# Optimization experiments

Hardware: AMD Instinct MI355X
Metric: run time of the kernel (lower is better)

## Reference

```python
import jax, jax.numpy as jnp
import numpy as np

MARGIN = 4.1
TOPK = 100          # argsort(...)[:100] in the original mining loop
NORM_EPS = 1e-8     # F.cosine_similarity eps
B, C, H, W = 4, 256, 64, 64


def setup_inputs() -> dict:
    key = jax.random.key(0)
    k1, k2, k3 = jax.random.split(key, 3)
    return {
        "sketch_query_vectors": jax.random.normal(k1, (B, C, H, W), jnp.float32),
        "ref_key_vectors": jax.random.normal(k2, (B, C, H, W), jnp.float32),
        "G": jax.random.uniform(k3, (B, H, W, 2), dtype=jnp.float32),  # normalized TPS grid
    }


def _forward(sketch, ref, G):
    Bq, Cq, Hq, Wq = sketch.shape
    HW = Hq * Wq
    scale = jnp.array([Wq, Hq], dtype=G.dtype)
    Gxy = G * scale  # pixel-space warp grid [B,H,W,2]

    # --- positive-pair selection (GridProcessing.get_positive, vectorized) ---
    x0 = jnp.floor(Gxy[..., 0]); y0 = jnp.floor(Gxy[..., 1])
    cx = jnp.stack([x0, x0 + 1.0, x0 + 1.0, x0], axis=-1)  # 4 bilinear corners [B,H,W,4]
    cy = jnp.stack([y0, y0, y0 + 1.0, y0 + 1.0], axis=-1)
    dists = jnp.sqrt((Gxy[..., 0:1] - cx) ** 2 + (Gxy[..., 1:2] - cy) ** 2)
    valid = (cx >= 0) & (cy >= 0) & (cx <= Wq - 1) & (cy <= Hq - 1)
    # original samples a corner with prob ~ max(d)+0.3-d; deterministic variant: take the
    # highest-probability (= nearest) in-bounds corner
    probs = jnp.where(valid, jnp.max(dists, axis=-1, keepdims=True) + 0.3 - dists, -jnp.inf)
    sel = jnp.argmax(probs, axis=-1)
    pair_valid = jnp.any(valid, axis=-1).reshape(Bq, HW)  # [B,P]
    ac_x = jnp.take_along_axis(cx, sel[..., None], -1)[..., 0].astype(jnp.int32)
    ac_y = jnp.take_along_axis(cy, sel[..., None], -1)[..., 0].astype(jnp.int32)
    ac_flat = jnp.clip((ac_y * Wq + ac_x).reshape(Bq, HW), 0, HW - 1)  # anchor index per pair

    # --- features & cosine distances ---
    sk = sketch.reshape(Bq, Cq, HW).transpose(0, 2, 1)  # [B,P,C]
    rf = ref.reshape(Bq, Cq, HW).transpose(0, 2, 1)     # [B,Q,C]
    nrm = lambda x: x / jnp.maximum(jnp.linalg.norm(x, axis=-1, keepdims=True), NORM_EPS)
    skn, rfn = nrm(sk), nrm(rf)
    anc = jnp.take_along_axis(skn, ac_flat[..., None], axis=1)  # anchor unit vecs [B,P,C]
    cos = jnp.einsum('bpc,bqc->bpq', anc, rfn)                  # [B,P,Q]
    d_neg = 1.0 - cos
    d_pos = jnp.diagonal(d_neg, axis1=1, axis2=2)               # positive = ref at pair index p
    losses = jax.nn.relu(d_pos[..., None] - d_neg + MARGIN)     # [B,P,Q]

    # --- hard-negative mining: 100 smallest losses (argsort()[:100]) ---
    _, negidx = jax.lax.top_k(-jax.lax.stop_gradient(losses), TOPK)  # [B,P,K]
    cand = jnp.take_along_axis(losses, negidx, axis=2)               # [B,P,K]

    # --- filtering (masked instead of ragged lists) ---
    keep = negidx != jnp.arange(HW)[None, :, None]              # drop the positive itself
    # original multiplies the (already pixel-scaled, mutated in-place) grid by scale again
    Graw = (Gxy * scale).reshape(Bq, HW, 2)
    neg_raw = jax.vmap(lambda g, i: g[i])(Graw, negidx)          # [B,P,K,2]
    diff = jnp.abs(neg_raw - Graw[:, :, None, :])
    keep = keep & ~((diff[..., 0] < 1.2) & (diff[..., 1] < 1.2))

    cnt = jnp.sum(keep, axis=-1).astype(losses.dtype)            # [B,P]
    per_pair = jnp.sum(jnp.where(keep, cand, 0.0), axis=-1) / jnp.maximum(cnt, 1.0)
    pair_valid = pair_valid & (cnt > 0)
    n = jnp.sum(pair_valid).astype(losses.dtype)
    return jnp.sum(jnp.where(pair_valid, per_pair, 0.0)) / (1e-6 + n)


def reference(sketch_query_vectors, ref_key_vectors, G):
    return _forward(sketch_query_vectors, ref_key_vectors, G)
```

## Files before the change

### kernel.cpp

```cpp
#include <hip/hip_runtime.h>

#define NB 4
#define NC 256
#define NHW 4096
#define NW 64
#define NTOPK 100
#define CAND 64
#define FMARGIN 4.1f

typedef float f32x4 __attribute__((ext_vector_type(4)));

__device__ __forceinline__ unsigned int tokey(float f) {
    unsigned int u = __float_as_uint(f);
    return (u & 0x80000000u) ? ~u : (u | 0x80000000u);
}
__device__ __forceinline__ float k16tof(unsigned int k) {
    unsigned int k32 = k << 16;
    return __uint_as_float((k32 & 0x80000000u) ? (k32 ^ 0x80000000u) : ~k32);
}

__global__ void k_pre(const float* __restrict__ sk, const float* __restrict__ rf,
                      const float* __restrict__ G,
                      int* __restrict__ ac_flat, int* __restrict__ pvalid,
                      unsigned char* __restrict__ refP, unsigned char* __restrict__ skT) {
    const int bid = blockIdx.x;
    if (bid < 64) {
        int t = bid * 256 + threadIdx.x;
        int b = t >> 12, p = t & (NHW - 1);
        float gxv = G[((size_t)b * NHW + p) * 2 + 0] * 64.0f;
        float gyv = G[((size_t)b * NHW + p) * 2 + 1] * 64.0f;
        float x0 = floorf(gxv), y0 = floorf(gyv);
        float cx[4] = {x0, x0 + 1.f, x0 + 1.f, x0};
        float cy[4] = {y0, y0, y0 + 1.f, y0 + 1.f};
        float d[4]; bool v[4]; float maxd = -INFINITY; bool any = false;
        #pragma unroll
        for (int i = 0; i < 4; ++i) {
            float dx = gxv - cx[i], dy = gyv - cy[i];
            d[i] = sqrtf(dx * dx + dy * dy);
            v[i] = (cx[i] >= 0.f) && (cy[i] >= 0.f) && (cx[i] <= 63.f) && (cy[i] <= 63.f);
            any = any || v[i];
            maxd = fmaxf(maxd, d[i]);
        }
        int sel = 0; float best = -INFINITY;
        #pragma unroll
        for (int i = 0; i < 4; ++i) {
            float prob = v[i] ? ((maxd + 0.3f) - d[i]) : -INFINITY;
            if (prob > best) { best = prob; sel = i; }
        }
        int acx = (int)cx[sel], acy = (int)cy[sel];
        int af = acy * NW + acx;
        af = af < 0 ? 0 : (af > NHW - 1 ? NHW - 1 : af);
        ac_flat[t] = af;
        pvalid[t] = any ? 1 : 0;
        return;
    }
    __shared__ float tile[64][NC + 1];
    __shared__ float psum[4][64];
    __shared__ float invs[64];
    const bool isB = bid < 320;
    const int blk = isB ? (bid - 64) : (bid - 320);
    const int b = blk >> 6;
    const int q0 = (blk & 63) << 6;
    const int t = threadIdx.x;
    const int qloc = t & 63;
    const int c0 = t >> 6;
    const float* base = (isB ? rf : sk) + (size_t)b * NC * NHW + q0 + qloc;
    #pragma unroll 8
    for (int cc = 0; cc < NC; cc += 4) {
        int c = cc + c0;
        tile[qloc][c] = base[(size_t)c * NHW];
    }
    __syncthreads();
    {
        float s = 0.f;
        #pragma unroll 8
        for (int j = 0; j < 64; ++j) { float v = tile[qloc][c0 * 64 + j]; s = fmaf(v, v, s); }
        psum[c0][qloc] = s;
    }
    __syncthreads();
    if (t < 64)
        invs[t] = 1.f / fmaxf(sqrtf(psum[0][t] + psum[1][t] + psum[2][t] + psum[3][t]), 1e-8f);
    __syncthreads();
    if (isB) {
        #pragma unroll
        for (int it = 0; it < 8; ++it) {
            int slot = it * 256 + t;
            int qt = slot >> 9;
            int kt = (slot >> 6) & 7;
            int lane = slot & 63;
            int g = lane >> 4, qll = lane & 15;
            int ql2 = (qt << 4) + qll;
            int c = kt * 32 + g * 8;
            const float iv = invs[ql2];
            unsigned int r0 = 0u, r1 = 0u;
            r0 = __builtin_amdgcn_cvt_pk_fp8_f32(tile[ql2][c + 0] * iv, tile[ql2][c + 1] * iv, r0, false);
            r0 = __builtin_amdgcn_cvt_pk_fp8_f32(tile[ql2][c + 2] * iv, tile[ql2][c + 3] * iv, r0, true);
            r1 = __builtin_amdgcn_cvt_pk_fp8_f32(tile[ql2][c + 4] * iv, tile[ql2][c + 5] * iv, r1, false);
            r1 = __builtin_amdgcn_cvt_pk_fp8_f32(tile[ql2][c + 6] * iv, tile[ql2][c + 7] * iv, r1, true);
            size_t oidx = (((size_t)(b * 256 + (q0 >> 4) + qt) * 8 + kt) * 64 + lane) * 8;
            *(uint2*)(refP + oidx) = make_uint2(r0, r1);
        }
    } else {
        const int row = t >> 2, seg = (t & 3) * 64;
        const float iv = invs[row];
        unsigned char* out = skT + ((size_t)b * NHW + q0 + row) * NC + seg;
        #pragma unroll
        for (int j0 = 0; j0 < 64; j0 += 8) {
            unsigned int r0 = 0u, r1 = 0u;
            r0 = __builtin_amdgcn_cvt_pk_fp8_f32(tile[row][seg + j0 + 0] * iv, tile[row][seg + j0 + 1] * iv, r0, false);
            r0 = __builtin_amdgcn_cvt_pk_fp8_f32(tile[row][seg + j0 + 2] * iv, tile[row][seg + j0 + 3] * iv, r0, true);
            r1 = __builtin_amdgcn_cvt_pk_fp8_f32(tile[row][seg + j0 + 4] * iv, tile[row][seg + j0 + 5] * iv, r1, false);
            r1 = __builtin_amdgcn_cvt_pk_fp8_f32(tile[row][seg + j0 + 6] * iv, tile[row][seg + j0 + 7] * iv, r1, true);
            *(uint2*)(out + j0) = make_uint2(r0, r1);
        }
    }
}

__global__ void k_part(const unsigned char* __restrict__ refP,
                       const unsigned char* __restrict__ skT,
                       const int* __restrict__ ac_flat,
                       float* __restrict__ cppg, unsigned int* __restrict__ cand) {
    __shared__ unsigned int key2q[8][1024];
    __shared__ __align__(16) unsigned char ancsA[8][64][8];

    const int tid = threadIdx.x;
    const int lane = tid & 63;
    const int w = tid >> 6;
    const int g = lane >> 4;
    const int ql = lane & 15;
    const int lblk = (blockIdx.x & 7) * 512 + (blockIdx.x >> 3);
    const int qtr = lblk & 3;
    const int rg = (lblk >> 2) & 255;
    const int b = lblk >> 10;
    const int p0 = rg << 4;

    if (tid < 256) {
        const int r = tid >> 4;
        const int ch = (tid & 15) << 4;
        const int a = ac_flat[b * NHW + p0 + r];
        uint4 v = *(const uint4*)(skT + ((size_t)b * NHW + a) * NC + ch);
        const int kk = ch >> 5;
        const int g1 = (ch >> 3) & 3;
        *(uint2*)&ancsA[kk][g1 * 16 + r][0] = make_uint2(v.x, v.y);
        *(uint2*)&ancsA[kk][(g1 + 1) * 16 + r][0] = make_uint2(v.z, v.w);
    }
    __syncthreads();

    long long af0 = *(const long long*)&ancsA[0][lane][0];
    long long af1 = *(const long long*)&ancsA[1][lane][0];
    long long af2 = *(const long long*)&ancsA[2][lane][0];
    long long af3 = *(const long long*)&ancsA[3][lane][0];
    long long af4 = *(const long long*)&ancsA[4][lane][0];
    long long af5 = *(const long long*)&ancsA[5][lane][0];
    long long af6 = *(const long long*)&ancsA[6][lane][0];
    long long af7 = *(const long long*)&ancsA[7][lane][0];

    const bool qDiag = (p0 >> 10) == qtr;
    const int tq = (p0 & 1023) >> 4;
    const int wstar = tq >> 3, tstar = tq & 7;

    #pragma unroll 2
    for (int t = 0; t < 8; ++t) {
        f32x4 a4 = (f32x4){0.f, 0.f, 0.f, 0.f};
        const unsigned char* bpt =
            refP + (((size_t)(b * 256 + qtr * 64 + w * 8 + t) * 8) * 64 + lane) * 8;
        a4 = __builtin_amdgcn_mfma_f32_16x16x32_fp8_fp8(af0, *(const long long*)(bpt + 0 * 512), a4, 0, 0, 0);
        a4 = __builtin_amdgcn_mfma_f32_16x16x32_fp8_fp8(af1, *(const long long*)(bpt + 1 * 512), a4, 0, 0, 0);
        a4 = __builtin_amdgcn_mfma_f32_16x16x32_fp8_fp8(af2, *(const long long*)(bpt + 2 * 512), a4, 0, 0, 0);
        a4 = __builtin_amdgcn_mfma_f32_16x16x32_fp8_fp8(af3, *(const long long*)(bpt + 3 * 512), a4, 0, 0, 0);
        a4 = __builtin_amdgcn_mfma_f32_16x16x32_fp8_fp8(af4, *(const long long*)(bpt + 4 * 512), a4, 0, 0, 0);
        a4 = __builtin_amdgcn_mfma_f32_16x16x32_fp8_fp8(af5, *(const long long*)(bpt + 5 * 512), a4, 0, 0, 0);
        a4 = __builtin_amdgcn_mfma_f32_16x16x32_fp8_fp8(af6, *(const long long*)(bpt + 6 * 512), a4, 0, 0, 0);
        a4 = __builtin_amdgcn_mfma_f32_16x16x32_fp8_fp8(af7, *(const long long*)(bpt + 7 * 512), a4, 0, 0, 0);
        if (qDiag && w == wstar && t == tstar) {
            #pragma unroll
            for (int i = 0; i < 4; ++i)
                if (ql == g * 4 + i) cppg[b * NHW + p0 + g * 4 + i] = a4[i];
        }
        unsigned int k01 = (tokey(a4[0]) >> 16) | ((tokey(a4[1]) >> 16) << 16);
        unsigned int k23 = (tokey(a4[2]) >> 16) | ((tokey(a4[3]) >> 16) << 16);
        const int ct = w * 8 + t;
        const int pos = (ql << 6) + (ct ^ ql);
        key2q[2 * g + 0][pos] = k01;
        key2q[2 * g + 1][pos] = k23;
    }
    __syncthreads();

    #pragma unroll 1
    for (int rr = 0; rr < 2; ++rr) {
        const int r = w * 2 + rr;
        const int rp = r >> 1;
        const int hsh = (r & 1) << 4;
        unsigned int ku[16];
        #pragma unroll
        for (int j = 0; j < 16; ++j)
            ku[j] = (key2q[rp][j * 64 + (lane ^ j)] >> hsh) & 0xFFFFu;

        unsigned int Ks = 0x4000u;
        int blw = 0;
        #pragma unroll 1
        for (int bit = 14; bit >= 0; --bit) {
            const unsigned int T = Ks | (1u << bit);
            int c = 0;
            #pragma unroll
            for (int j = 0; j < 16; ++j)
                c += __popcll(__ballot(ku[j] < T));
            if (c < CAND) { Ks = T; blw = c; }
        }
        const int tk = CAND - blw;

        int nlt = 0, ltc = 0;
        #pragma unroll
        for (int j = 0; j < 16; ++j) {
            nlt += (ku[j] < Ks) ? 1 : 0;
            ltc += (ku[j] == Ks) ? 1 : 0;
        }
        int packed = nlt | (ltc << 16);
        int pscan = packed;
        #pragma unroll
        for (int d = 1; d < 64; d <<= 1) {
            int t2 = __shfl_up(pscan, d, 64);
            if (lane >= d) pscan += t2;
        }
        pscan -= packed;
        const int nltpfx = pscan & 0xFFFF;
        const int tpfx = pscan >> 16;

        unsigned int* crow = cand + ((size_t)(b * NHW + p0 + r)) * 256 + qtr * CAND;
        int si = 0, mt = 0;
        #pragma unroll
        for (int j = 0; j < 16; ++j) {
            const unsigned int gc = (unsigned)(qtr * 1024 + lane * 16 + j);
            if (ku[j] < Ks) {
                crow[nltpfx + si] = (ku[j] << 12) | gc;
                si++;
            } else if (ku[j] == Ks) {
                if (tpfx + mt < tk) crow[blw + tpfx + mt] = (Ks << 12) | gc;
                mt++;
            }
        }
    }
}

__global__ void k_merge(const unsigned int* __restrict__ cand, const float* __restrict__ cppg,
                        const float* __restrict__ G, const int* __restrict__ pvalid,
                        float* __restrict__ row_val, int* __restrict__ row_valid) {
    const int lane = threadIdx.x & 63;
    const int w = threadIdx.x >> 6;
    const int row = blockIdx.x * 8 + w;
    const int b = row >> 12;
    const int pg = row & 4095;
    uint4 v = *(const uint4*)&cand[(size_t)row * 256 + lane * 4];
    unsigned int pk[4] = {v.x, v.y, v.z, v.w};

    unsigned int Ks = 0x4000u << 12;
    #pragma unroll 1
    for (int bit = 25; bit >= 0; --bit) {
        const unsigned int T = Ks | (1u << bit);
        int c = 0;
        #pragma unroll
        for (int j = 0; j < 4; ++j)
            c += __popcll(__ballot(pk[j] < T));
        if (c < NTOPK) Ks = T;
    }

    const float dpos = 1.0f - cppg[row];
    const float2 gp = *(const float2*)&G[(size_t)row * 2];
    const float px = gp.x * 4096.f, py = gp.y * 4096.f;
    const float base_add = dpos + (FMARGIN - 1.0f);

    float fl = 0.f; int ccnt = 0;
    #pragma unroll
    for (int j = 0; j < 4; ++j) {
        if (pk[j] <= Ks) {
            const int q = (int)(pk[j] & 4095u);
            bool keep = (q != pg);
            if (keep) {
                float2 g2 = *(const float2*)&G[((size_t)(b * NHW + q)) * 2];
                float dx = fabsf(g2.x * 4096.f - px), dy = fabsf(g2.y * 4096.f - py);
                keep = !((dx < 1.2f) && (dy < 1.2f));
            }
            if (keep) { fl += base_add + k16tof(pk[j] >> 12); ccnt++; }
        }
    }
    #pragma unroll
    for (int d = 1; d < 64; d <<= 1) {
        fl += __shfl_xor(fl, d, 64);
        ccnt += __shfl_xor(ccnt, d, 64);
    }
    if (lane == 0) {
        const int pv = (pvalid[row] != 0) && (ccnt > 0);
        row_val[row] = pv ? (fl / (float)ccnt) : 0.f;
        row_valid[row] = pv;
    }
}

__global__ __attribute__((amdgpu_flat_work_group_size(1024, 1024), amdgpu_waves_per_eu(4, 4)))
void k_main_r12(const unsigned char* __restrict__ refP, const unsigned char* __restrict__ skT,
                const float* __restrict__ G,
                const int* __restrict__ ac_flat, const int* __restrict__ pvalid,
                float* __restrict__ row_val, int* __restrict__ row_valid)
{
    __shared__ unsigned int key2[8][NHW];
    __shared__ __align__(16) unsigned char ancsA[8][64][8];
    __shared__ float cpp[16];

    const int tid = threadIdx.x;
    const int lane = tid & 63;
    const int w = tid >> 6;
    const int g = lane >> 4;
    const int ql = lane & 15;
    const int lblk = (blockIdx.x & 7) * 128 + (blockIdx.x >> 3);
    const int b = lblk >> 8;
    const int p0 = (lblk & 255) << 4;

    {
        const int a = ac_flat[b * NHW + p0 + w];
        const unsigned char* src = skT + ((size_t)b * NHW + a) * NC;
        unsigned int v = *(const unsigned int*)(src + lane * 4);
        const int c = lane * 4;
        const int kk = c >> 5, gg = (c >> 3) & 3, j = c & 7;
        *(unsigned int*)&ancsA[kk][gg * 16 + w][j] = v;
    }
    __syncthreads();

    const int wstar = p0 >> 8;
    const int tstar = (p0 >> 4) & 15;
    long long af0 = *(const long long*)&ancsA[0][lane][0];
    long long af1 = *(const long long*)&ancsA[1][lane][0];
    long long af2 = *(const long long*)&ancsA[2][lane][0];
    long long af3 = *(const long long*)&ancsA[3][lane][0];
    long long af4 = *(const long long*)&ancsA[4][lane][0];
    long long af5 = *(const long long*)&ancsA[5][lane][0];
    long long af6 = *(const long long*)&ancsA[6][lane][0];
    long long af7 = *(const long long*)&ancsA[7][lane][0];

    #pragma unroll 4
    for (int t = 0; t < 16; ++t) {
        f32x4 a4 = (f32x4){0.f, 0.f, 0.f, 0.f};
        const unsigned char* bpt =
            refP + (((size_t)(b * 256 + w * 16 + t) * 8) * 64 + lane) * 8;
        a4 = __builtin_amdgcn_mfma_f32_16x16x32_fp8_fp8(af0, *(const long long*)(bpt + 0 * 512), a4, 0, 0, 0);
        a4 = __builtin_amdgcn_mfma_f32_16x16x32_fp8_fp8(af1, *(const long long*)(bpt + 1 * 512), a4, 0, 0, 0);
        a4 = __builtin_amdgcn_mfma_f32_16x16x32_fp8_fp8(af2, *(const long long*)(bpt + 2 * 512), a4, 0, 0, 0);
        a4 = __builtin_amdgcn_mfma_f32_16x16x32_fp8_fp8(af3, *(const long long*)(bpt + 3 * 512), a4, 0, 0, 0);
        a4 = __builtin_amdgcn_mfma_f32_16x16x32_fp8_fp8(af4, *(const long long*)(bpt + 4 * 512), a4, 0, 0, 0);
        a4 = __builtin_amdgcn_mfma_f32_16x16x32_fp8_fp8(af5, *(const long long*)(bpt + 5 * 512), a4, 0, 0, 0);
        a4 = __builtin_amdgcn_mfma_f32_16x16x32_fp8_fp8(af6, *(const long long*)(bpt + 6 * 512), a4, 0, 0, 0);
        a4 = __builtin_amdgcn_mfma_f32_16x16x32_fp8_fp8(af7, *(const long long*)(bpt + 7 * 512), a4, 0, 0, 0);
        if (w == wstar && t == tstar) {
            #pragma unroll
            for (int i = 0; i < 4; ++i)
                if (ql == g * 4 + i) cpp[g * 4 + i] = a4[i];
        }
        unsigned int k01 = (tokey(a4[0]) >> 16) | ((tokey(a4[1]) >> 16) << 16);
        unsigned int k23 = (tokey(a4[2]) >> 16) | ((tokey(a4[3]) >> 16) << 16);
        const int l_r = (w << 2) + (t >> 2);
        const int ach = ((t & 3) << 2) + (ql >> 2);
        const int pidx = (l_r << 6) + ((ach ^ (l_r & 15)) << 2) + (ql & 3);
        key2[(g << 1) + 0][pidx] = k01;
        key2[(g << 1) + 1][pidx] = k23;
    }
    __syncthreads();

    const int rp = w >> 1;
    const int half = w & 1;
    unsigned int ku[64];
    #pragma unroll
    for (int ach = 0; ach < 16; ++ach) {
        const uint4 v = *(const uint4*)&key2[rp][(lane << 6) + ((ach ^ (lane & 15)) << 2)];
        ku[4 * ach + 0] = half ? (v.x >> 16) : (v.x & 0xFFFFu);
        ku[4 * ach + 1] = half ? (v.y >> 16) : (v.y & 0xFFFFu);
        ku[4 * ach + 2] = half ? (v.z >> 16) : (v.z & 0xFFFFu);
        ku[4 * ach + 3] = half ? (v.w >> 16) : (v.w & 0xFFFFu);
    }
    unsigned int Ks = 0x4000u;
    #pragma unroll 1
    for (int bit = 14; bit >= 0; --bit) {
        const unsigned int T = Ks | (1u << bit);
        int c = 0;
        #pragma unroll
        for (int j = 0; j < 64; ++j)
            c += __popcll(__ballot(ku[j] < T));
        if (c < NTOPK) Ks = T;
    }
    int below = 0;
    #pragma unroll
    for (int j = 0; j < 64; ++j)
        below += __popcll(__ballot(ku[j] < Ks));
    const int tk = NTOPK - below;

    const float dpos = 1.0f - cpp[w];
    const int pg = p0 + w;
    const float2 gp = *(const float2*)&G[((size_t)b * NHW + pg) * 2];
    const float px = gp.x * 4096.f, py = gp.y * 4096.f;
    const float base_add = dpos + (FMARGIN - 1.0f);

    float sumv = 0.f; int cnt = 0;
    unsigned long long tmask = 0ull; int ltc = 0;
    #pragma unroll
    for (int j = 0; j < 64; ++j) {
        const unsigned int k = ku[j];
        if (k < Ks) {
            const int q = (lane << 6) + 8 * (j >> 2) + 2 * (j & 3) + half;
            bool keep = (q != pg);
            if (keep) {
                float2 g2 = *(const float2*)&G[((size_t)b * NHW + q) * 2];
                float dx = fabsf(g2.x * 4096.f - px), dy = fabsf(g2.y * 4096.f - py);
                keep = !((dx < 1.2f) && (dy < 1.2f));
            }
            if (keep) { sumv += k16tof(k); cnt++; }
        } else if (k == Ks) {
            tmask |= (1ull << j);
            ltc++;
        }
    }
    int pfx = ltc;
    #pragma unroll
    for (int d = 1; d < 64; d <<= 1) {
        int t2 = __shfl_up(pfx, d, 64);
        if (lane >= d) pfx += t2;
    }
    pfx -= ltc;
    int ek = 0;
    if (ltc > 0 && pfx < tk) {
        unsigned long long mm = tmask;
        int m = 0;
        while (mm) {
            const int j = __ffsll((unsigned long long)mm) - 1;
            mm &= mm - 1;
            if (pfx + m < tk) {
                const int q = (lane << 6) + 8 * (j >> 2) + 2 * (j & 3) + half;
                bool keep = (q != pg);
                if (keep) {
                    float2 g2 = *(const float2*)&G[((size_t)b * NHW + q) * 2];
                    float dx = fabsf(g2.x * 4096.f - px), dy = fabsf(g2.y * 4096.f - py);
                    keep = !((dx < 1.2f) && (dy < 1.2f));
                }
                if (keep) ek++;
            }
            m++;
        }
    }
    const float vstar = k16tof(Ks);
    float fl = sumv + (float)cnt * base_add + (float)ek * (base_add + vstar);
    int ccnt = cnt + ek;
    #pragma unroll
    for (int d = 1; d < 64; d <<= 1) {
        fl += __shfl_xor(fl, d, 64);
        ccnt += __shfl_xor(ccnt, d, 64);
    }
    if (lane == 0) {
        const int pv = (pvalid[b * NHW + pg] != 0) && (ccnt > 0);
        row_val[b * NHW + pg] = pv ? (fl / (float)ccnt) : 0.f;
        row_valid[b * NHW + pg] = pv;
    }
}

__global__ void k_reduce(const float* __restrict__ row_val, const int* __restrict__ row_valid,
                         float* __restrict__ out) {
    __shared__ float ss[1024];
    __shared__ int sc[1024];
    float s = 0.f; int n = 0;
    for (int i = threadIdx.x; i < NB * NHW; i += 1024) { s += row_val[i]; n += row_valid[i]; }
    ss[threadIdx.x] = s; sc[threadIdx.x] = n;
    __syncthreads();
    for (int d = 512; d > 0; d >>= 1) {
        if (threadIdx.x < d) { ss[threadIdx.x] += ss[threadIdx.x + d]; sc[threadIdx.x] += sc[threadIdx.x + d]; }
        __syncthreads();
    }
    if (threadIdx.x == 0) out[0] = ss[0] / (1e-6f + (float)sc[0]);
}

extern "C" void kernel_launch(void* const* d_in, const int* in_sizes, int n_in,
                              void* d_out, int out_size, void* d_ws, size_t ws_size,
                              hipStream_t stream) {
    const float* sk = (const float*)d_in[0];
    const float* rf = (const float*)d_in[1];
    const float* G  = (const float*)d_in[2];
    char* ws = (char*)d_ws;
    const size_t SMALL5 = 5ull * 65536ull;
    const size_t PANEL8 = (size_t)NB * NC * NHW;
    const size_t CANDSZ = (size_t)NB * NHW * 256 * 4;
    const size_t QNEED = SMALL5 + 2 * PANEL8 + CANDSZ;
    int*   ac   = (int*)  (ws + 0 * 65536);
    int*   pv   = (int*)  (ws + 1 * 65536);
    float* rv_  = (float*)(ws + 2 * 65536);
    int*   rvd  = (int*)  (ws + 3 * 65536);
    float* cppg = (float*)(ws + 4 * 65536);
    unsigned char* rf8 = (unsigned char*)(ws + SMALL5);
    unsigned char* sk8 = (unsigned char*)(ws + SMALL5 + PANEL8);
    unsigned int* cand = (unsigned int*)(ws + SMALL5 + 2 * PANEL8);

    hipLaunchKernelGGL(k_pre, dim3(576), dim3(256), 0, stream,
                       sk, rf, G, ac, pv, rf8, sk8);
    if (ws_size >= QNEED) {
        hipLaunchKernelGGL(k_part, dim3(4096), dim3(512), 0, stream,
                           rf8, sk8, ac, cppg, cand);
        hipLaunchKernelGGL(k_merge, dim3(2048), dim3(512), 0, stream,
                           cand, cppg, G, pv, rv_, rvd);
    } else {
        hipLaunchKernelGGL(k_main_r12, dim3(1024), dim3(1024), 0, stream,
                           rf8, sk8, G, ac, pv, rv_, rvd);
    }
    hipLaunchKernelGGL(k_reduce, dim3(1), dim3(1024), 0, stream, rv_, rvd, (float*)d_out);
}
```

Measured before the change: 146.6 us.

## Split partial top-k into eighths of Q with 32 candidates each

```diff
diff --git a/kernel.cpp b/kernel.cpp
--- a/kernel.cpp
+++ b/kernel.cpp
@@ -5,7 +5,7 @@
 #define NHW 4096
 #define NW 64
 #define NTOPK 100
-#define CAND 64
+#define CANDE 32
 #define FMARGIN 4.1f
 
 typedef float f32x4 __attribute__((ext_vector_type(4)));
@@ -120,7 +120,7 @@
                        const unsigned char* __restrict__ skT,
                        const int* __restrict__ ac_flat,
                        float* __restrict__ cppg, unsigned int* __restrict__ cand) {
-    __shared__ unsigned int key2q[8][1024];
+    __shared__ unsigned int key2e[8][520];
     __shared__ __align__(16) unsigned char ancsA[8][64][8];
 
     const int tid = threadIdx.x;
@@ -128,10 +128,10 @@
     const int w = tid >> 6;
     const int g = lane >> 4;
     const int ql = lane & 15;
-    const int lblk = (blockIdx.x & 7) * 512 + (blockIdx.x >> 3);
-    const int qtr = lblk & 3;
-    const int rg = (lblk >> 2) & 255;
-    const int b = lblk >> 10;
+    const int lblk = (blockIdx.x & 7) * 1024 + (blockIdx.x >> 3);
+    const int e = lblk & 7;
+    const int rg = (lblk >> 3) & 255;
+    const int b = lblk >> 11;
     const int p0 = rg << 4;
 
     if (tid < 256) {
@@ -155,15 +155,15 @@
     long long af6 = *(const long long*)&ancsA[6][lane][0];
     long long af7 = *(const long long*)&ancsA[7][lane][0];
 
-    const bool qDiag = (p0 >> 10) == qtr;
-    const int tq = (p0 & 1023) >> 4;
-    const int wstar = tq >> 3, tstar = tq & 7;
-
-    #pragma unroll 2
-    for (int t = 0; t < 8; ++t) {
+    const bool eDiag = (p0 >> 9) == e;
+    const int tq = (p0 & 511) >> 4;
+    const int wstar = tq >> 2, tstar = tq & 3;
+
+    #pragma unroll
+    for (int t = 0; t < 4; ++t) {
         f32x4 a4 = (f32x4){0.f, 0.f, 0.f, 0.f};
         const unsigned char* bpt =
-            refP + (((size_t)(b * 256 + qtr * 64 + w * 8 + t) * 8) * 64 + lane) * 8;
+            refP + (((size_t)(b * 256 + e * 32 + w * 4 + t) * 8) * 64 + lane) * 8;
         a4 = __builtin_amdgcn_mfma_f32_16x16x32_fp8_fp8(af0, *(const long long*)(bpt + 0 * 512), a4, 0, 0, 0);
         a4 = __builtin_amdgcn_mfma_f32_16x16x32_fp8_fp8(af1, *(const long long*)(bpt + 1 * 512), a4, 0, 0, 0);
         a4 = __builtin_amdgcn_mfma_f32_16x16x32_fp8_fp8(af2, *(const long long*)(bpt + 2 * 512), a4, 0, 0, 0);
@@ -172,17 +172,17 @@
         a4 = __builtin_amdgcn_mfma_f32_16x16x32_fp8_fp8(af5, *(const long long*)(bpt + 5 * 512), a4, 0, 0, 0);
         a4 = __builtin_amdgcn_mfma_f32_16x16x32_fp8_fp8(af6, *(const long long*)(bpt + 6 * 512), a4, 0, 0, 0);
         a4 = __builtin_amdgcn_mfma_f32_16x16x32_fp8_fp8(af7, *(const long long*)(bpt + 7 * 512), a4, 0, 0, 0);
-        if (qDiag && w == wstar && t == tstar) {
+        if (eDiag && w == wstar && t == tstar) {
             #pragma unroll
             for (int i = 0; i < 4; ++i)
                 if (ql == g * 4 + i) cppg[b * NHW + p0 + g * 4 + i] = a4[i];
         }
         unsigned int k01 = (tokey(a4[0]) >> 16) | ((tokey(a4[1]) >> 16) << 16);
         unsigned int k23 = (tokey(a4[2]) >> 16) | ((tokey(a4[3]) >> 16) << 16);
-        const int ct = w * 8 + t;
-        const int pos = (ql << 6) + (ct ^ ql);
-        key2q[2 * g + 0][pos] = k01;
-        key2q[2 * g + 1][pos] = k23;
+        const int ct = w * 4 + t;
+        const int pos = (ql << 5) + (ct ^ ql);
+        key2e[2 * g + 0][pos] = k01;
+        key2e[2 * g + 1][pos] = k23;
     }
     __syncthreads();
 
@@ -191,10 +191,12 @@
         const int r = w * 2 + rr;
         const int rp = r >> 1;
         const int hsh = (r & 1) << 4;
-        unsigned int ku[16];
-        #pragma unroll
-        for (int j = 0; j < 16; ++j)
-            ku[j] = (key2q[rp][j * 64 + (lane ^ j)] >> hsh) & 0xFFFFu;
+        unsigned int ku[8];
+        #pragma unroll
+        for (int j = 0; j < 8; ++j) {
+            const int c = lane * 8 + j;
+            ku[j] = (key2e[rp][((c & 15) << 5) + ((c >> 4) ^ (c & 15))] >> hsh) & 0xFFFFu;
+        }
 
         unsigned int Ks = 0x4000u;
         int blw = 0;
@@ -203,15 +205,15 @@
             const unsigned int T = Ks | (1u << bit);
             int c = 0;
             #pragma unroll
-            for (int j = 0; j < 16; ++j)
+            for (int j = 0; j < 8; ++j)
                 c += __popcll(__ballot(ku[j] < T));
-            if (c < CAND) { Ks = T; blw = c; }
-        }
-        const int tk = CAND - blw;
+            if (c < CANDE) { Ks = T; blw = c; }
+        }
+        const int tk = CANDE - blw;
 
         int nlt = 0, ltc = 0;
         #pragma unroll
-        for (int j = 0; j < 16; ++j) {
+        for (int j = 0; j < 8; ++j) {
             nlt += (ku[j] < Ks) ? 1 : 0;
             ltc += (ku[j] == Ks) ? 1 : 0;
         }
@@ -226,11 +228,11 @@
         const int nltpfx = pscan & 0xFFFF;
         const int tpfx = pscan >> 16;
 
-        unsigned int* crow = cand + ((size_t)(b * NHW + p0 + r)) * 256 + qtr * CAND;
+        unsigned int* crow = cand + ((size_t)(b * NHW + p0 + r)) * 256 + e * CANDE;
         int si = 0, mt = 0;
         #pragma unroll
-        for (int j = 0; j < 16; ++j) {
-            const unsigned int gc = (unsigned)(qtr * 1024 + lane * 16 + j);
+        for (int j = 0; j < 8; ++j) {
+            const unsigned int gc = (unsigned)(e * 512 + lane * 8 + j);
             if (ku[j] < Ks) {
                 crow[nltpfx + si] = (ku[j] << 12) | gc;
                 si++;
@@ -495,7 +497,7 @@
     hipLaunchKernelGGL(k_pre, dim3(576), dim3(256), 0, stream,
                        sk, rf, G, ac, pv, rf8, sk8);
     if (ws_size >= QNEED) {
-        hipLaunchKernelGGL(k_part, dim3(4096), dim3(512), 0, stream,
+        hipLaunchKernelGGL(k_part, dim3(8192), dim3(512), 0, stream,
                            rf8, sk8, ac, cppg, cand);
         hipLaunchKernelGGL(k_merge, dim3(2048), dim3(512), 0, stream,
                            cand, cppg, G, pv, rv_, rvd);
```

Measured after the change: 148.7 us. Within noise of the previous version (+1.5%).
